# Performance work log

Hardware: AMD Instinct MI355X
Metric: run time of the kernel (lower is better)

## Reference

```python
import jax, jax.numpy as jnp
from jax import lax
import numpy as np

N = 8192
E = 131072
HID = 256
ENC = 256
L = 4
EPS = 1e-5


def _linear(x, w, b):
    return x @ w.T + b


def _layernorm(x, g, b):
    mu = x.mean(-1, keepdims=True)
    var = ((x - mu) ** 2).mean(-1, keepdims=True)
    return (x - mu) / jnp.sqrt(var + EPS) * g + b


def _conv_bn_gelu(x, w, b, g, beta, stride, pad):
    # eval-mode BatchNorm with running_mean=0, running_var=1
    y = lax.conv_general_dilated(x, w, (stride, stride), [(pad, pad), (pad, pad)],
                                 dimension_numbers=('NCHW', 'OIHW', 'NCHW'))
    y = y + b[None, :, None, None]
    y = y / jnp.sqrt(1.0 + EPS) * g[None, :, None, None] + beta[None, :, None, None]
    return jax.nn.gelu(y, approximate=False)


def setup_inputs() -> dict:
    key = jax.random.key(0)
    ks = iter(jax.random.split(key, 40))

    def rn(shape, scale=0.05):
        return (jax.random.normal(next(ks), shape, jnp.float32) * scale)

    inp = {
        'patches': jax.random.normal(next(ks), (N, 3, 32, 32), jnp.float32),
        'coords': jax.random.uniform(next(ks), (N, 2), jnp.float32) * 10000.0,
        'edge_index': jax.random.randint(next(ks), (2, E), 0, N),
        # SimpleCNNEncoder
        'c1_w': rn((32, 3, 5, 5)), 'c1_b': rn((32,)), 'bn1_g': jnp.ones((32,)), 'bn1_b': jnp.zeros((32,)),
        'c2_w': rn((64, 32, 3, 3)), 'c2_b': rn((64,)), 'bn2_g': jnp.ones((64,)), 'bn2_b': jnp.zeros((64,)),
        'c3_w': rn((128, 64, 3, 3)), 'c3_b': rn((128,)), 'bn3_g': jnp.ones((128,)), 'bn3_b': jnp.zeros((128,)),
        'c4_w': rn((256, 128, 3, 3)), 'c4_b': rn((256,)), 'bn4_g': jnp.ones((256,)), 'bn4_b': jnp.zeros((256,)),
        'enc_proj_w': rn((ENC, 256)), 'enc_proj_b': rn((ENC,)),
        # projector
        'pj_w': rn((HID, ENC + 2)), 'pj_b': rn((HID,)),
        'pln_g': jnp.ones((HID,)), 'pln_b': jnp.zeros((HID,)),
        # graph blocks (stacked over L)
        'gb_msg_w': rn((L, HID, HID)), 'gb_msg_b': rn((L, HID)),
        'gb_sp_w': rn((L, HID, HID)), 'gb_sp_b': rn((L, HID)),
        'gb_ln_g': jnp.ones((L, HID)), 'gb_ln_b': jnp.zeros((L, HID)),
        # heads
        'comp_w': rn((8, HID)), 'comp_b': rn((8,)),
        'cmpo_w': rn((16, HID)), 'cmpo_b': rn((16,)),
        'prog_w': rn((32, HID)), 'prog_b': rn((32,)),
    }
    return inp


def _forward(patches, coords, edge_index,
             c1_w, c1_b, bn1_g, bn1_b, c2_w, c2_b, bn2_g, bn2_b,
             c3_w, c3_b, bn3_g, bn3_b, c4_w, c4_b, bn4_g, bn4_b,
             enc_proj_w, enc_proj_b, pj_w, pj_b, pln_g, pln_b,
             gb_msg_w, gb_msg_b, gb_sp_w, gb_sp_b, gb_ln_g, gb_ln_b,
             comp_w, comp_b, cmpo_w, cmpo_b, prog_w, prog_b):
    # CNN encoder
    h = _conv_bn_gelu(patches, c1_w, c1_b, bn1_g, bn1_b, 2, 2)   # [N,32,16,16]
    h = _conv_bn_gelu(h, c2_w, c2_b, bn2_g, bn2_b, 2, 1)         # [N,64,8,8]
    h = _conv_bn_gelu(h, c3_w, c3_b, bn3_g, bn3_b, 2, 1)         # [N,128,4,4]
    h = _conv_bn_gelu(h, c4_w, c4_b, bn4_g, bn4_b, 2, 1)         # [N,256,2,2]
    h = h.mean(axis=(2, 3))                                       # AdaptiveAvgPool2d(1)
    img_feat = _linear(h, enc_proj_w, enc_proj_b)                 # [N,ENC]

    # projector (Dropout is identity in eval)
    x = jnp.concatenate([img_feat, coords / 10000.0], axis=1)
    x = _layernorm(_linear(x, pj_w, pj_b), pln_g, pln_b)
    x = jax.nn.gelu(x, approximate=False)

    # graph blocks: gather -> linear -> scatter-mean -> residual -> LN
    src, dst = edge_index[0], edge_index[1]
    n = x.shape[0]
    deg = jax.ops.segment_sum(jnp.ones_like(dst, x.dtype), dst, num_segments=n)
    inv_deg = 1.0 / jnp.maximum(deg, 1.0)
    for i in range(gb_msg_w.shape[0]):
        messages = _linear(x[src], gb_msg_w[i], gb_msg_b[i])      # [E,HID]
        agg = jax.ops.segment_sum(messages, dst, num_segments=n) * inv_deg[:, None]
        out = _linear(x, gb_sp_w[i], gb_sp_b[i]) + agg
        x = _layernorm(x + jax.nn.gelu(out, approximate=False), gb_ln_g[i], gb_ln_b[i])

    return (x,
            _linear(x, comp_w, comp_b),
            _linear(x, cmpo_w, cmpo_b),
            _linear(x, prog_w, prog_b))


def reference(patches, coords, edge_index,
              c1_w, c1_b, bn1_g, bn1_b, c2_w, c2_b, bn2_g, bn2_b,
              c3_w, c3_b, bn3_g, bn3_b, c4_w, c4_b, bn4_g, bn4_b,
              enc_proj_w, enc_proj_b, pj_w, pj_b, pln_g, pln_b,
              gb_msg_w, gb_msg_b, gb_sp_w, gb_sp_b, gb_ln_g, gb_ln_b,
              comp_w, comp_b, cmpo_w, cmpo_b, prog_w, prog_b):
    return _forward(patches, coords, edge_index,
                    c1_w, c1_b, bn1_g, bn1_b, c2_w, c2_b, bn2_g, bn2_b,
                    c3_w, c3_b, bn3_g, bn3_b, c4_w, c4_b, bn4_g, bn4_b,
                    enc_proj_w, enc_proj_b, pj_w, pj_b, pln_g, pln_b,
                    gb_msg_w, gb_msg_b, gb_sp_w, gb_sp_b, gb_ln_g, gb_ln_b,
                    comp_w, comp_b, cmpo_w, cmpo_b, prog_w, prog_b)
```

## Files before the change

### kernel.cpp

```cpp
#include <hip/hip_runtime.h>
#include <hip/hip_bf16.h>

#define N_ 8192
#define E_ 131072

typedef unsigned short u16;
typedef unsigned int u32;
typedef __attribute__((ext_vector_type(8))) short bf16x8;
typedef __attribute__((ext_vector_type(4))) float f32x4;

__device__ __forceinline__ float bf2f(u16 u){ return __uint_as_float(((u32)u)<<16); }
__device__ __forceinline__ u16 f2bf(float f){
  u32 u = __float_as_uint(f);
  u32 r = (u + 0x7fffu + ((u>>16)&1u)) >> 16;
  return (u16)r;
}
__device__ __forceinline__ float gelu_f(float x){ return 0.5f*x*(1.f+erff(x*0.70710678118654752f)); }

template<int S1,int S2>
__device__ __forceinline__ u32 swz(u32 b){
  if (S1==0) return b;
  u32 k = b >> S1;
  if (S2) k ^= (b >> S2);
  return b ^ ((k & 7u) << 4);
}

__global__ __launch_bounds__(256) void wpack1_k(const float* __restrict__ src,
    u16* __restrict__ dst)
{
  int e = blockIdx.x*256 + threadIdx.x;
  if (e < 3328){
    int co = e / 104, r = e - co*104;
    int ci = r >> 5, tap = r & 31;
    u16 v = 0;
    if (ci < 3 && tap < 25) v = f2bf(src[co*75 + ci*25 + tap]);
    dst[e] = v;
  }
}

__global__ __launch_bounds__(256) void wpack_k(const float* __restrict__ src,
    u16* __restrict__ dst, int CO, int CI, int total)
{
  int e = blockIdx.x*256 + threadIdx.x;
  if (e < total){
    int tap = e / (CO*CI);
    int rem = e - tap*CO*CI;
    int co = rem / CI, ci = rem - co*CI;
    dst[e] = f2bf(src[((size_t)co*CI + ci)*9 + tap]);
  }
}

__global__ __launch_bounds__(256) void conv1m_k(const float* __restrict__ patches,
    const u16* __restrict__ wp, const float* __restrict__ cb,
    const float* __restrict__ bng, const float* __restrict__ bnb,
    u16* __restrict__ h1)
{
  __shared__ __align__(16) u16 sbuf[4000 + 3328];
  int t = threadIdx.x;
  int img = blockIdx.x;

  for (int e=t; e<2000; e+=256) ((u32*)sbuf)[e] = 0;
  {
    const uint4* s4 = (const uint4*)wp;
    uint4* d4 = (uint4*)(sbuf + 4000);
    for (int e=t; e<416; e+=256) d4[e] = s4[e];
  }
  __syncthreads();
  {
    const float* src = patches + (size_t)img*3072;
    for (int e=t; e<3072; e+=256){
      int ci = e >> 10, rem = e & 1023, iy = rem >> 5, ix = rem & 31;
      sbuf[ci*1332 + (iy+2)*37 + (ix+2)] = f2bf(src[e]);
    }
  }
  __syncthreads();

  int lane = t & 63, wv = t >> 6;
  int lr = lane & 15, g = lane >> 4;

  int roff[8];
  #pragma unroll
  for (int j=0;j<8;++j){
    int tap = g*8 + j;
    int ty = (tap*13) >> 6;
    int tx = tap - ty*5;
    roff[j] = ty*74 + tx*2;
  }

  int pixb[4];
  #pragma unroll
  for (int mt=0;mt<4;++mt){
    int row = wv*64 + mt*16 + lr;
    int oy = row >> 4, ox = row & 15;
    pixb[mt] = oy*148 + ox*4;
  }

  f32x4 acc[4][2];
  #pragma unroll
  for (int mt=0;mt<4;++mt){
    acc[mt][0] = (f32x4){0.f,0.f,0.f,0.f};
    acc[mt][1] = (f32x4){0.f,0.f,0.f,0.f};
  }

  #pragma unroll
  for (int ks=0; ks<3; ++ks){
    bf16x8 bfr[2];
    #pragma unroll
    for (int nt=0;nt<2;++nt){
      u32 b = (u32)((nt*16+lr)*208 + ks*64 + g*16);
      bfr[nt] = *(const bf16x8*)((const char*)(sbuf+4000) + b);
    }
    #pragma unroll
    for (int mt=0;mt<4;++mt){
      union { bf16x8 v; u16 s[8]; } a;
      const char* base = (const char*)sbuf + ks*2664 + pixb[mt];
      #pragma unroll
      for (int j=0;j<8;++j) a.s[j] = *(const u16*)(base + roff[j]);
      acc[mt][0] = __builtin_amdgcn_mfma_f32_16x16x32_bf16(a.v, bfr[0], acc[mt][0], 0,0,0);
      acc[mt][1] = __builtin_amdgcn_mfma_f32_16x16x32_bf16(a.v, bfr[1], acc[mt][1], 0,0,0);
    }
  }

  #pragma unroll
  for (int nt=0;nt<2;++nt){
    int co = nt*16 + lr;
    float S = bng[co]*rsqrtf(1.f+1e-5f);
    float T = cb[co]*S + bnb[co];
    #pragma unroll
    for (int mt=0;mt<4;++mt){
      #pragma unroll
      for (int j=0;j<4;++j){
        int opix = wv*64 + mt*16 + g*4 + j;
        h1[(size_t)img*8192 + opix*32 + co] = f2bf(gelu_f(acc[mt][nt][j]*S + T));
      }
    }
  }
}

template<int CI,int CO,int IH,int OH,int WAVES,int MT,int SA1,int SA2,int POOL>
__global__ __launch_bounds__(WAVES*64) void convm_k(const u16* __restrict__ hin,
    const u16* __restrict__ wp, const float* __restrict__ cb,
    const float* __restrict__ bng, const float* __restrict__ bnb,
    u16* __restrict__ hout, float* __restrict__ pooled)
{
  constexpr int OPIX = OH*OH, IPIX = IH*IH;
  constexpr int NT = CO/16, KS = CI/32;
  constexpr int ROWS = WAVES*MT*16;
  constexpr int IMG = ROWS/OPIX;
  constexpr int IMGB = IPIX*CI*2;
  constexpr int TH = WAVES*64;
  constexpr int OPSH = (OPIX==64)?6:((OPIX==16)?4:2);
  constexpr int OHSH = (OH==8)?3:((OH==4)?2:1);

  __shared__ u16 in_l[IMG*IPIX*CI];

  int t = threadIdx.x, blk = blockIdx.x;
  int lane = t & 63, wv = t >> 6;
  int lr = lane & 15, g = lane >> 4;

  {
    const uint4* src = (const uint4*)(hin + (size_t)blk*IMG*IPIX*CI);
    constexpr int CH = IMG*IPIX*CI/8;
    for (int e=t; e<CH; e+=TH){
      uint4 v = src[e];
      *(uint4*)((char*)in_l + swz<SA1,SA2>((u32)e*16u)) = v;
    }
  }
  __syncthreads();

  int oyv[MT], oxv[MT], ibv[MT];
  #pragma unroll
  for (int mt=0; mt<MT; ++mt){
    int rl = wv*(MT*16) + mt*16 + lr;
    int imgl = rl >> OPSH;
    int opix = rl & (OPIX-1);
    oyv[mt] = opix >> OHSH;
    oxv[mt] = opix & (OH-1);
    ibv[mt] = imgl*IMGB;
  }

  f32x4 acc[MT][NT];
  #pragma unroll
  for (int mt=0;mt<MT;++mt)
    #pragma unroll
    for (int nt=0;nt<NT;++nt) acc[mt][nt] = (f32x4){0.f,0.f,0.f,0.f};

  for (int tap=0; tap<9; ++tap){
    int ky = (tap<3)?0:((tap<6)?1:2);
    int kx = tap - ky*3;
    const u16* wt = wp + (size_t)tap*CO*CI;
    #pragma unroll
    for (int ks=0; ks<KS; ++ks){
      bf16x8 af[MT];
      #pragma unroll
      for (int mt=0; mt<MT; ++mt){
        int iy = 2*oyv[mt] - 1 + ky;
        int ix = 2*oxv[mt] - 1 + kx;
        bf16x8 a = {};
        if (iy>=0 && iy<IH && ix>=0 && ix<IH){
          u32 b = (u32)(ibv[mt] + (iy*IH+ix)*CI*2 + ks*64 + g*16);
          a = *(const bf16x8*)((const char*)in_l + swz<SA1,SA2>(b));
        }
        af[mt] = a;
      }
      #pragma unroll
      for (int nt=0; nt<NT; ++nt){
        bf16x8 bfr = *(const bf16x8*)(wt + (size_t)(nt*16+lr)*CI + ks*32 + g*8);
        #pragma unroll
        for (int mt=0; mt<MT; ++mt)
          acc[mt][nt] = __builtin_amdgcn_mfma_f32_16x16x32_bf16(af[mt], bfr, acc[mt][nt], 0, 0, 0);
      }
    }
  }

  if (!POOL){
    #pragma unroll
    for (int nt=0; nt<NT; ++nt){
      int co = nt*16 + lr;
      float S = bng[co]*rsqrtf(1.f+1e-5f);
      float T = cb[co]*S + bnb[co];
      #pragma unroll
      for (int mt=0; mt<MT; ++mt){
        #pragma unroll
        for (int j=0;j<4;++j){
          int rl = wv*(MT*16) + mt*16 + g*4 + j;
          int imgl = rl >> OPSH, opix = rl & (OPIX-1);
          float y = gelu_f(acc[mt][nt][j]*S + T);
          hout[((size_t)(blk*IMG + imgl)*OPIX + opix)*CO + co] = f2bf(y);
        }
      }
    }
  } else {
    #pragma unroll
    for (int nt=0; nt<NT; ++nt){
      int co = nt*16 + lr;
      float S = bng[co]*rsqrtf(1.f+1e-5f);
      float T = cb[co]*S + bnb[co];
      float s = 0.f;
      #pragma unroll
      for (int j=0;j<4;++j) s += gelu_f(acc[0][nt][j]*S + T);
      int n = blk*IMG + wv*4 + g;
      pooled[(size_t)n*CO + co] = 0.25f*s;
    }
  }
}

template<int MODE>
__global__ __launch_bounds__(256) void gemm_k(const float* __restrict__ A, const float* __restrict__ W,
   const float* __restrict__ bias, int ldw,
   const float* __restrict__ A2, const float* __restrict__ W2, const float* __restrict__ bias2,
   const int* __restrict__ deg, const float* __restrict__ coords, const float* __restrict__ pjw,
   float* __restrict__ C)
{
  __shared__ float a_l[32*16];
  __shared__ float b_l[32*256];
  int t=threadIdx.x; int row0=blockIdx.x*16;
  int tm=t>>6, tn=t&63;
  float acc[4][4];
  #pragma unroll
  for (int i=0;i<4;++i)
    #pragma unroll
    for (int j=0;j<4;++j) acc[i][j]=0.f;
  const int passes = (MODE==2)?2:1;
  for (int ps2=0; ps2<passes; ++ps2){
    const float* Ap = ps2? A2:A; const float* Wp = ps2? W2:W; int ld = ps2?256:ldw;
    for (int k0=0;k0<256;k0+=32){
      {
        int e=t*2; int r=e>>5; int k=e&31;
        float2 v = *(const float2*)&Ap[(size_t)(row0+r)*256 + k0+k];
        a_l[k*16+r]=v.x; a_l[(k+1)*16+r]=v.y;
      }
      {
        const float* wr = &Wp[(size_t)t*ld + k0];
        #pragma unroll
        for (int kk=0;kk<32;kk+=2){ float2 v = *(const float2*)&wr[kk]; b_l[kk*256+t]=v.x; b_l[(kk+1)*256+t]=v.y; }
      }
      __syncthreads();
      #pragma unroll
      for (int k=0;k<32;++k){
        float4 av = *(const float4*)&a_l[k*16+tm*4];
        float4 bv = *(const float4*)&b_l[k*256+tn*4];
        float aa[4]={av.x,av.y,av.z,av.w};
        float bb[4]={bv.x,bv.y,bv.z,bv.w};
        #pragma unroll
        for (int i=0;i<4;++i)
          #pragma unroll
          for (int j=0;j<4;++j) acc[i][j]+=aa[i]*bb[j];
      }
      __syncthreads();
    }
  }
  float4 bv = *(const float4*)&bias[tn*4];
  float bias4[4]={bv.x,bv.y,bv.z,bv.w};
  float b24[4]={0.f,0.f,0.f,0.f};
  float cw0[4], cw1[4];
  if (MODE==2){
    float4 b2 = *(const float4*)&bias2[tn*4];
    b24[0]=b2.x; b24[1]=b2.y; b24[2]=b2.z; b24[3]=b2.w;
  }
  if (MODE==1){
    #pragma unroll
    for (int j=0;j<4;++j){ cw0[j]=pjw[(size_t)(tn*4+j)*258+256]; cw1[j]=pjw[(size_t)(tn*4+j)*258+257]; }
  }
  #pragma unroll
  for (int i=0;i<4;++i){
    int r = row0 + tm*4 + i;
    float g2 = 0.f, c0=0.f, c1=0.f;
    if (MODE==2) g2 = (deg[r]>0)?1.f:0.f;
    if (MODE==1){ c0 = coords[(size_t)r*2]*1e-4f; c1 = coords[(size_t)r*2+1]*1e-4f; }
    float4 o;
    float vals[4];
    #pragma unroll
    for (int j=0;j<4;++j){
      float v = acc[i][j] + bias4[j];
      if (MODE==2) v += g2*b24[j];
      if (MODE==1) v += c0*cw0[j] + c1*cw1[j];
      vals[j]=v;
    }
    o.x=vals[0]; o.y=vals[1]; o.z=vals[2]; o.w=vals[3];
    *(float4*)&C[(size_t)r*256 + tn*4] = o;
  }
}

template<int MODE>
__global__ __launch_bounds__(256) void ln_k(const float* __restrict__ xin, const float* __restrict__ tin,
  const float* __restrict__ g, const float* __restrict__ b, float* __restrict__ out)
{
  int row = blockIdx.x, t = threadIdx.x;
  size_t o = (size_t)row*256+t;
  float v;
  if (MODE==0) v = tin[o];
  else v = xin[o] + gelu_f(tin[o]);
  float s = v, sq = v*v;
  #pragma unroll
  for (int off=32; off>=1; off>>=1){ s += __shfl_xor(s,off); sq += __shfl_xor(sq,off); }
  __shared__ float red[8];
  int wv = t>>6;
  if ((t&63)==0){ red[wv*2]=s; red[wv*2+1]=sq; }
  __syncthreads();
  s = red[0]+red[2]+red[4]+red[6];
  sq = red[1]+red[3]+red[5]+red[7];
  float mu = s*(1.f/256.f);
  float var = sq*(1.f/256.f) - mu*mu;
  float rs = rsqrtf(var + 1e-5f);
  float y = (v-mu)*rs*g[t] + b[t];
  if (MODE==0) y = gelu_f(y);
  out[o] = y;
}

__global__ __launch_bounds__(256) void degcount_k(const int* __restrict__ dst, int* __restrict__ deg){
  int e = blockIdx.x*256+threadIdx.x;
  if (e<E_) atomicAdd(&deg[dst[e]],1);
}

__global__ __launch_bounds__(256) void scan_k(const int* __restrict__ deg, int* __restrict__ rowptr,
  float* __restrict__ invd)
{
  __shared__ int part[256];
  int t = threadIdx.x;
  int base = t*32; int run=0; int loc[32];
  #pragma unroll
  for (int i=0;i<32;++i){ loc[i]=run; run += deg[base+i]; }
  part[t]=run;
  __syncthreads();
  for (int off=1; off<256; off<<=1){
    int v = (t>=off)? part[t-off] : 0;
    __syncthreads();
    part[t]+=v;
    __syncthreads();
  }
  int pre = (t>0)? part[t-1] : 0;
  #pragma unroll
  for (int i=0;i<32;++i){
    rowptr[base+i] = pre + loc[i];
    int dv = deg[base+i];
    invd[base+i] = 1.f/fmaxf((float)dv,1.f);
  }
  if (t==255) rowptr[N_] = part[255];
}

__global__ __launch_bounds__(256) void fill_k(const int* __restrict__ src, const int* __restrict__ dst,
  const int* __restrict__ rowptr, int* __restrict__ cursor, int* __restrict__ colidx)
{
  int e = blockIdx.x*256+threadIdx.x;
  if (e<E_){
    int d = dst[e];
    int pos = rowptr[d] + atomicAdd(&cursor[d],1);
    colidx[pos] = src[e];
  }
}

__global__ __launch_bounds__(256) void gather_k(const float* __restrict__ x, const int* __restrict__ rowptr,
    const int* __restrict__ colidx, const float* __restrict__ invd, float* __restrict__ xbar)
{
  int d = blockIdx.x, t = threadIdx.x;
  int j0 = rowptr[d], j1 = rowptr[d+1];
  float s = 0.f;
  for (int j=j0;j<j1;++j){ int c = colidx[j]; s += x[(size_t)c*256+t]; }
  xbar[(size_t)d*256+t] = s*invd[d];
}

__global__ __launch_bounds__(64) void heads_k(const float* __restrict__ x,
  const float* __restrict__ cw, const float* __restrict__ cbs,
  const float* __restrict__ mw, const float* __restrict__ mbs,
  const float* __restrict__ pw, const float* __restrict__ pbs,
  float* __restrict__ out)
{
  __shared__ float xr[256];
  int row = blockIdx.x, t = threadIdx.x;
  *(float4*)&xr[t*4] = *(const float4*)&x[(size_t)row*256 + t*4];
  __syncthreads();
  if (t>=56) return;
  const float* w; float bb; float* op;
  if (t<8){ w=&cw[t*256]; bb=cbs[t]; op = out + 2097152 + (size_t)row*8 + t; }
  else if (t<24){ int q=t-8; w=&mw[q*256]; bb=mbs[q]; op = out + 2162688 + (size_t)row*16 + q; }
  else { int q=t-24; w=&pw[q*256]; bb=pbs[q]; op = out + 2293760 + (size_t)row*32 + q; }
  float acc=0.f;
  #pragma unroll 8
  for (int k=0;k<256;k+=4){
    float4 xv=*(const float4*)&xr[k];
    float4 wv=*(const float4*)&w[k];
    acc += xv.x*wv.x + xv.y*wv.y + xv.z*wv.z + xv.w*wv.w;
  }
  *op = acc + bb;
}

extern "C" void kernel_launch(void* const* d_in, const int* in_sizes, int n_in,
                              void* d_out, int out_size, void* d_ws, size_t ws_size,
                              hipStream_t stream)
{
  const float* patches = (const float*)d_in[0];
  const float* coords  = (const float*)d_in[1];
  const int*   eidx    = (const int*)d_in[2];
  const float* c1w = (const float*)d_in[3];  const float* c1b = (const float*)d_in[4];
  const float* b1g = (const float*)d_in[5];  const float* b1b = (const float*)d_in[6];
  const float* c2w = (const float*)d_in[7];  const float* c2b = (const float*)d_in[8];
  const float* b2g = (const float*)d_in[9];  const float* b2b = (const float*)d_in[10];
  const float* c3w = (const float*)d_in[11]; const float* c3b = (const float*)d_in[12];
  const float* b3g = (const float*)d_in[13]; const float* b3b = (const float*)d_in[14];
  const float* c4w = (const float*)d_in[15]; const float* c4b = (const float*)d_in[16];
  const float* b4g = (const float*)d_in[17]; const float* b4b = (const float*)d_in[18];
  const float* encw = (const float*)d_in[19]; const float* encb = (const float*)d_in[20];
  const float* pjw  = (const float*)d_in[21]; const float* pjb  = (const float*)d_in[22];
  const float* plng = (const float*)d_in[23]; const float* plnb = (const float*)d_in[24];
  const float* msgw = (const float*)d_in[25]; const float* msgb = (const float*)d_in[26];
  const float* spw  = (const float*)d_in[27]; const float* spb  = (const float*)d_in[28];
  const float* lng  = (const float*)d_in[29]; const float* lnb  = (const float*)d_in[30];
  const float* compw = (const float*)d_in[31]; const float* compb = (const float*)d_in[32];
  const float* cmpow = (const float*)d_in[33]; const float* cmpob = (const float*)d_in[34];
  const float* progw = (const float*)d_in[35]; const float* progb = (const float*)d_in[36];
  float* out = (float*)d_out;
  char* ws = (char*)d_ws;

  const size_t OFF_H1   = 0;
  const size_t OFF_H2   = 134217728;
  const size_t OFF_H3   = 201326592;
  const size_t OFF_POOL = 234881024;
  const size_t OFF_IMGF = 243269632;
  const size_t OFF_TBUF = 251658240;
  const size_t OFF_XA   = 260046848;
  const size_t OFF_XB   = 268435456;
  const size_t OFF_XBAR = 276824064;
  const size_t OFF_DEG  = 285212672;
  const size_t OFF_ROWP = 285245440;
  const size_t OFF_CURS = 285310976;
  const size_t OFF_COL  = 285343744;
  const size_t OFF_INVD = 285868032;
  const size_t OFF_WP4  = OFF_TBUF;
  const size_t OFF_WP3  = OFF_TBUF + 589824;
  const size_t OFF_WP2  = OFF_TBUF + 737280;
  const size_t OFF_WP1  = OFF_TBUF + 774144;

  u16* h1 = (u16*)(ws+OFF_H1);
  u16* h2 = (u16*)(ws+OFF_H2);
  u16* h3 = (u16*)(ws+OFF_H3);
  float* pooled = (float*)(ws+OFF_POOL);
  float* imgf = (float*)(ws+OFF_IMGF);
  float* tbuf = (float*)(ws+OFF_TBUF);
  float* xa = (float*)(ws+OFF_XA);
  float* xb = (float*)(ws+OFF_XB);
  float* xbar = (float*)(ws+OFF_XBAR);
  int* deg = (int*)(ws+OFF_DEG);
  int* rowp = (int*)(ws+OFF_ROWP);
  int* curs = (int*)(ws+OFF_CURS);
  int* col = (int*)(ws+OFF_COL);
  float* invd = (float*)(ws+OFF_INVD);
  u16* wp1 = (u16*)(ws+OFF_WP1);
  u16* wp2 = (u16*)(ws+OFF_WP2);
  u16* wp3 = (u16*)(ws+OFF_WP3);
  u16* wp4 = (u16*)(ws+OFF_WP4);

  hipMemsetAsync(deg, 0, 32768, stream);
  hipMemsetAsync(curs, 0, 32768, stream);

  wpack1_k<<<13,256,0,stream>>>(c1w, wp1);
  wpack_k<<<(18432+255)/256,256,0,stream>>>(c2w, wp2, 64, 32, 18432);
  wpack_k<<<(73728+255)/256,256,0,stream>>>(c3w, wp3, 128, 64, 73728);
  wpack_k<<<(294912+255)/256,256,0,stream>>>(c4w, wp4, 256, 128, 294912);

  conv1m_k<<<8192,256,0,stream>>>(patches, wp1, c1b, b1g, b1b, h1);
  convm_k<32,64,16,8,8,2,7,0,0><<<2048,512,0,stream>>>(h1, wp2, c2b, b2g, b2b, h2, nullptr);
  convm_k<64,128,8,4,4,2,8,11,0><<<1024,256,0,stream>>>(h2, wp3, c3b, b3g, b3b, h3, nullptr);
  convm_k<128,256,4,2,8,1,9,12,1><<<256,512,0,stream>>>(h3, wp4, c4b, b4g, b4b, nullptr, pooled);

  gemm_k<0><<<512,256,0,stream>>>(pooled, encw, encb, 256, nullptr,nullptr,nullptr,nullptr,nullptr,nullptr, imgf);
  gemm_k<1><<<512,256,0,stream>>>(imgf, pjw, pjb, 258, nullptr,nullptr,nullptr,nullptr, coords, pjw, tbuf);
  ln_k<0><<<8192,256,0,stream>>>(tbuf, tbuf, plng, plnb, xa);

  degcount_k<<<512,256,0,stream>>>(eidx+E_, deg);
  scan_k<<<1,256,0,stream>>>(deg, rowp, invd);
  fill_k<<<512,256,0,stream>>>(eidx, eidx+E_, rowp, curs, col);

  float* xcur = xa;
  for (int i=0;i<4;++i){
    gather_k<<<8192,256,0,stream>>>(xcur, rowp, col, invd, xbar);
    gemm_k<2><<<512,256,0,stream>>>(xcur, spw+(size_t)i*65536, spb+(size_t)i*256, 256,
                                    xbar, msgw+(size_t)i*65536, msgb+(size_t)i*256,
                                    deg, nullptr, nullptr, tbuf);
    float* xnext = (i==3)? out : ((i&1)? xa : xb);
    ln_k<1><<<8192,256,0,stream>>>(xcur, tbuf, lng+(size_t)i*256, lnb+(size_t)i*256, xnext);
    xcur = xnext;
  }
  heads_k<<<8192,64,0,stream>>>(out, compw, compb, cmpow, cmpob, progw, progb, out);
}
```

Baseline: 1.068 ms.

## Move dense linears to bf16 MFMA and split conv output channels across waves

Replaces the fp32 SIMT GEMM for the encoder projection, projector and graph-block linears with a bf16 MFMA GEMM tiled 64x64 over a 2D grid. Weights are pre-packed to bf16, and activations (pooled, imgf, x, xbar) get bf16 copies written by the producing kernels. The conv3 and conv4 kernels now split output channels across waves, which doubles their grid sizes for more parallelism. This trades fp32 precision in the graph GEMMs for tensor-core throughput, adds extra bf16 stores in the layernorm kernel, and adds weight-packing launches.

Result: faster. 947.5 us (-11.3%).

```diff
diff --git a/kernel.cpp b/kernel.cpp
--- a/kernel.cpp
+++ b/kernel.cpp
@@ -50,6 +50,16 @@
   }
 }
 
+__global__ __launch_bounds__(256) void wpackg_k(const float* __restrict__ src,
+    u16* __restrict__ dst, int ld, int total)
+{
+  int e = blockIdx.x*256 + threadIdx.x;
+  if (e < total){
+    int co = e >> 8, k = e & 255;
+    dst[e] = f2bf(src[(size_t)co*ld + k]);
+  }
+}
+
 __global__ __launch_bounds__(256) void conv1m_k(const float* __restrict__ patches,
     const u16* __restrict__ wp, const float* __restrict__ cb,
     const float* __restrict__ bng, const float* __restrict__ bnb,
@@ -137,26 +147,30 @@
   }
 }
 
-template<int CI,int CO,int IH,int OH,int WAVES,int MT,int SA1,int SA2,int POOL>
+template<int CI,int CO,int IH,int OH,int WAVES,int NW,int MT,int SA1,int SA2,int POOL>
 __global__ __launch_bounds__(WAVES*64) void convm_k(const u16* __restrict__ hin,
     const u16* __restrict__ wp, const float* __restrict__ cb,
     const float* __restrict__ bng, const float* __restrict__ bnb,
-    u16* __restrict__ hout, float* __restrict__ pooled)
+    u16* __restrict__ hout, u16* __restrict__ pooled)
 {
   constexpr int OPIX = OH*OH, IPIX = IH*IH;
-  constexpr int NT = CO/16, KS = CI/32;
-  constexpr int ROWS = WAVES*MT*16;
+  constexpr int NT = CO/16/NW, KS = CI/32;
+  constexpr int MG = WAVES/NW;
+  constexpr int ROWS = MG*MT*16;
   constexpr int IMG = ROWS/OPIX;
   constexpr int IMGB = IPIX*CI*2;
   constexpr int TH = WAVES*64;
   constexpr int OPSH = (OPIX==64)?6:((OPIX==16)?4:2);
   constexpr int OHSH = (OH==8)?3:((OH==4)?2:1);
+  constexpr int NWS = (NW==1)?0:((NW==2)?1:2);
 
   __shared__ u16 in_l[IMG*IPIX*CI];
 
   int t = threadIdx.x, blk = blockIdx.x;
   int lane = t & 63, wv = t >> 6;
   int lr = lane & 15, g = lane >> 4;
+  int mg = wv >> NWS, nw = wv & (NW-1);
+  int ncb = nw*(NT*16);
 
   {
     const uint4* src = (const uint4*)(hin + (size_t)blk*IMG*IPIX*CI);
@@ -171,7 +185,7 @@
   int oyv[MT], oxv[MT], ibv[MT];
   #pragma unroll
   for (int mt=0; mt<MT; ++mt){
-    int rl = wv*(MT*16) + mt*16 + lr;
+    int rl = mg*(MT*16) + mt*16 + lr;
     int imgl = rl >> OPSH;
     int opix = rl & (OPIX-1);
     oyv[mt] = opix >> OHSH;
@@ -205,7 +219,7 @@
       }
       #pragma unroll
       for (int nt=0; nt<NT; ++nt){
-        bf16x8 bfr = *(const bf16x8*)(wt + (size_t)(nt*16+lr)*CI + ks*32 + g*8);
+        bf16x8 bfr = *(const bf16x8*)(wt + (size_t)(ncb + nt*16+lr)*CI + ks*32 + g*8);
         #pragma unroll
         for (int mt=0; mt<MT; ++mt)
           acc[mt][nt] = __builtin_amdgcn_mfma_f32_16x16x32_bf16(af[mt], bfr, acc[mt][nt], 0, 0, 0);
@@ -216,14 +230,14 @@
   if (!POOL){
     #pragma unroll
     for (int nt=0; nt<NT; ++nt){
-      int co = nt*16 + lr;
+      int co = ncb + nt*16 + lr;
       float S = bng[co]*rsqrtf(1.f+1e-5f);
       float T = cb[co]*S + bnb[co];
       #pragma unroll
       for (int mt=0; mt<MT; ++mt){
         #pragma unroll
         for (int j=0;j<4;++j){
-          int rl = wv*(MT*16) + mt*16 + g*4 + j;
+          int rl = mg*(MT*16) + mt*16 + g*4 + j;
           int imgl = rl >> OPSH, opix = rl & (OPIX-1);
           float y = gelu_f(acc[mt][nt][j]*S + T);
           hout[((size_t)(blk*IMG + imgl)*OPIX + opix)*CO + co] = f2bf(y);
@@ -233,98 +247,83 @@
   } else {
     #pragma unroll
     for (int nt=0; nt<NT; ++nt){
-      int co = nt*16 + lr;
+      int co = ncb + nt*16 + lr;
       float S = bng[co]*rsqrtf(1.f+1e-5f);
       float T = cb[co]*S + bnb[co];
-      float s = 0.f;
-      #pragma unroll
-      for (int j=0;j<4;++j) s += gelu_f(acc[0][nt][j]*S + T);
-      int n = blk*IMG + wv*4 + g;
-      pooled[(size_t)n*CO + co] = 0.25f*s;
+      #pragma unroll
+      for (int mt=0; mt<MT; ++mt){
+        float s = 0.f;
+        #pragma unroll
+        for (int j=0;j<4;++j) s += gelu_f(acc[mt][nt][j]*S + T);
+        int n = blk*IMG + mg*(MT*4) + mt*4 + g;
+        pooled[(size_t)n*CO + co] = f2bf(0.25f*s);
+      }
     }
   }
 }
 
 template<int MODE>
-__global__ __launch_bounds__(256) void gemm_k(const float* __restrict__ A, const float* __restrict__ W,
-   const float* __restrict__ bias, int ldw,
-   const float* __restrict__ A2, const float* __restrict__ W2, const float* __restrict__ bias2,
-   const int* __restrict__ deg, const float* __restrict__ coords, const float* __restrict__ pjw,
-   float* __restrict__ C)
-{
-  __shared__ float a_l[32*16];
-  __shared__ float b_l[32*256];
-  int t=threadIdx.x; int row0=blockIdx.x*16;
-  int tm=t>>6, tn=t&63;
-  float acc[4][4];
-  #pragma unroll
-  for (int i=0;i<4;++i)
-    #pragma unroll
-    for (int j=0;j<4;++j) acc[i][j]=0.f;
+__global__ __launch_bounds__(256) void gemm_m(
+    const u16* __restrict__ A1, const u16* __restrict__ W1, const float* __restrict__ b1,
+    const u16* __restrict__ A2, const u16* __restrict__ W2, const float* __restrict__ b2,
+    const int* __restrict__ deg, const float* __restrict__ coords, const float* __restrict__ pjw,
+    float* __restrict__ Cf, u16* __restrict__ Ch)
+{
+  __shared__ __align__(16) u16 a_l[64*256];
+  int t=threadIdx.x, lane=t&63, w=t>>6, lr=lane&15, g=lane>>4;
+  int m0 = blockIdx.x*64, n0 = blockIdx.y*64;
+
+  f32x4 acc[4];
+  #pragma unroll
+  for (int nt=0;nt<4;++nt) acc[nt] = (f32x4){0.f,0.f,0.f,0.f};
+
   const int passes = (MODE==2)?2:1;
-  for (int ps2=0; ps2<passes; ++ps2){
-    const float* Ap = ps2? A2:A; const float* Wp = ps2? W2:W; int ld = ps2?256:ldw;
-    for (int k0=0;k0<256;k0+=32){
-      {
-        int e=t*2; int r=e>>5; int k=e&31;
-        float2 v = *(const float2*)&Ap[(size_t)(row0+r)*256 + k0+k];
-        a_l[k*16+r]=v.x; a_l[(k+1)*16+r]=v.y;
+  for (int ps=0; ps<passes; ++ps){
+    const u16* Ap = ps? A2:A1;
+    const u16* Wp = ps? W2:W1;
+    __syncthreads();
+    for (int e=t; e<2048; e+=256){
+      u32 b = (u32)e*16u;
+      uint4 v = *(const uint4*)(Ap + (size_t)(m0 + (e>>5))*256 + (e&31)*8);
+      *(uint4*)((char*)a_l + (b ^ (((b>>9)&7u)<<4))) = v;
+    }
+    __syncthreads();
+    #pragma unroll
+    for (int ks=0; ks<8; ++ks){
+      u32 ab = (u32)(w*16+lr)*512 + (u32)ks*64 + (u32)g*16;
+      bf16x8 af = *(const bf16x8*)((const char*)a_l + (ab ^ (((ab>>9)&7u)<<4)));
+      #pragma unroll
+      for (int nt=0; nt<4; ++nt){
+        bf16x8 bfv = *(const bf16x8*)(Wp + (size_t)(n0+nt*16+lr)*256 + ks*32 + g*8);
+        acc[nt] = __builtin_amdgcn_mfma_f32_16x16x32_bf16(af, bfv, acc[nt], 0,0,0);
       }
-      {
-        const float* wr = &Wp[(size_t)t*ld + k0];
-        #pragma unroll
-        for (int kk=0;kk<32;kk+=2){ float2 v = *(const float2*)&wr[kk]; b_l[kk*256+t]=v.x; b_l[(kk+1)*256+t]=v.y; }
-      }
-      __syncthreads();
-      #pragma unroll
-      for (int k=0;k<32;++k){
-        float4 av = *(const float4*)&a_l[k*16+tm*4];
-        float4 bv = *(const float4*)&b_l[k*256+tn*4];
-        float aa[4]={av.x,av.y,av.z,av.w};
-        float bb[4]={bv.x,bv.y,bv.z,bv.w};
-        #pragma unroll
-        for (int i=0;i<4;++i)
-          #pragma unroll
-          for (int j=0;j<4;++j) acc[i][j]+=aa[i]*bb[j];
-      }
-      __syncthreads();
-    }
-  }
-  float4 bv = *(const float4*)&bias[tn*4];
-  float bias4[4]={bv.x,bv.y,bv.z,bv.w};
-  float b24[4]={0.f,0.f,0.f,0.f};
-  float cw0[4], cw1[4];
-  if (MODE==2){
-    float4 b2 = *(const float4*)&bias2[tn*4];
-    b24[0]=b2.x; b24[1]=b2.y; b24[2]=b2.z; b24[3]=b2.w;
-  }
-  if (MODE==1){
-    #pragma unroll
-    for (int j=0;j<4;++j){ cw0[j]=pjw[(size_t)(tn*4+j)*258+256]; cw1[j]=pjw[(size_t)(tn*4+j)*258+257]; }
-  }
-  #pragma unroll
-  for (int i=0;i<4;++i){
-    int r = row0 + tm*4 + i;
-    float g2 = 0.f, c0=0.f, c1=0.f;
-    if (MODE==2) g2 = (deg[r]>0)?1.f:0.f;
-    if (MODE==1){ c0 = coords[(size_t)r*2]*1e-4f; c1 = coords[(size_t)r*2+1]*1e-4f; }
-    float4 o;
-    float vals[4];
+    }
+  }
+
+  int row_base = m0 + w*16 + g*4;
+  #pragma unroll
+  for (int nt=0; nt<4; ++nt){
+    int col = n0 + nt*16 + lr;
+    float bb = b1[col];
+    float b2v = 0.f, cw0 = 0.f, cw1 = 0.f;
+    if (MODE==2) b2v = b2[col];
+    if (MODE==1){ cw0 = pjw[(size_t)col*258+256]; cw1 = pjw[(size_t)col*258+257]; }
     #pragma unroll
     for (int j=0;j<4;++j){
-      float v = acc[i][j] + bias4[j];
-      if (MODE==2) v += g2*b24[j];
-      if (MODE==1) v += c0*cw0[j] + c1*cw1[j];
-      vals[j]=v;
-    }
-    o.x=vals[0]; o.y=vals[1]; o.z=vals[2]; o.w=vals[3];
-    *(float4*)&C[(size_t)r*256 + tn*4] = o;
+      int r = row_base + j;
+      float v = acc[nt][j] + bb;
+      if (MODE==2) v += (deg[r]>0)? b2v : 0.f;
+      if (MODE==1) v += coords[(size_t)r*2]*1e-4f*cw0 + coords[(size_t)r*2+1]*1e-4f*cw1;
+      if (MODE==0) Ch[(size_t)r*256 + col] = f2bf(v);
+      else         Cf[(size_t)r*256 + col] = v;
+    }
   }
 }
 
 template<int MODE>
 __global__ __launch_bounds__(256) void ln_k(const float* __restrict__ xin, const float* __restrict__ tin,
-  const float* __restrict__ g, const float* __restrict__ b, float* __restrict__ out)
+  const float* __restrict__ g, const float* __restrict__ b, float* __restrict__ out,
+  u16* __restrict__ houtb)
 {
   int row = blockIdx.x, t = threadIdx.x;
   size_t o = (size_t)row*256+t;
@@ -346,6 +345,7 @@
   float y = (v-mu)*rs*g[t] + b[t];
   if (MODE==0) y = gelu_f(y);
   out[o] = y;
+  houtb[o] = f2bf(y);
 }
 
 __global__ __launch_bounds__(256) void degcount_k(const int* __restrict__ dst, int* __restrict__ deg){
@@ -391,13 +391,13 @@
 }
 
 __global__ __launch_bounds__(256) void gather_k(const float* __restrict__ x, const int* __restrict__ rowptr,
-    const int* __restrict__ colidx, const float* __restrict__ invd, float* __restrict__ xbar)
+    const int* __restrict__ colidx, const float* __restrict__ invd, u16* __restrict__ xbarh)
 {
   int d = blockIdx.x, t = threadIdx.x;
   int j0 = rowptr[d], j1 = rowptr[d+1];
   float s = 0.f;
   for (int j=j0;j<j1;++j){ int c = colidx[j]; s += x[(size_t)c*256+t]; }
-  xbar[(size_t)d*256+t] = s*invd[d];
+  xbarh[(size_t)d*256+t] = f2bf(s*invd[d]);
 }
 
 __global__ __launch_bounds__(64) void heads_k(const float* __restrict__ x,
@@ -460,7 +460,6 @@
   const size_t OFF_TBUF = 251658240;
   const size_t OFF_XA   = 260046848;
   const size_t OFF_XB   = 268435456;
-  const size_t OFF_XBAR = 276824064;
   const size_t OFF_DEG  = 285212672;
   const size_t OFF_ROWP = 285245440;
   const size_t OFF_CURS = 285310976;
@@ -470,16 +469,21 @@
   const size_t OFF_WP3  = OFF_TBUF + 589824;
   const size_t OFF_WP2  = OFF_TBUF + 737280;
   const size_t OFF_WP1  = OFF_TBUF + 774144;
+  const size_t OFF_ENCH = OFF_POOL + 4194304;
+  const size_t OFF_PJH  = OFF_POOL + 4325376;
+  const size_t OFF_SPH  = OFF_IMGF + 4194304;
+  const size_t OFF_MSGH = OFF_IMGF + 4718592;
+  const size_t OFF_XH   = OFF_H1;
+  const size_t OFF_XBH  = OFF_H1 + 4194304;
 
   u16* h1 = (u16*)(ws+OFF_H1);
   u16* h2 = (u16*)(ws+OFF_H2);
   u16* h3 = (u16*)(ws+OFF_H3);
-  float* pooled = (float*)(ws+OFF_POOL);
-  float* imgf = (float*)(ws+OFF_IMGF);
+  u16* pooled = (u16*)(ws+OFF_POOL);
+  u16* imgf_h = (u16*)(ws+OFF_IMGF);
   float* tbuf = (float*)(ws+OFF_TBUF);
   float* xa = (float*)(ws+OFF_XA);
   float* xb = (float*)(ws+OFF_XB);
-  float* xbar = (float*)(ws+OFF_XBAR);
   int* deg = (int*)(ws+OFF_DEG);
   int* rowp = (int*)(ws+OFF_ROWP);
   int* curs = (int*)(ws+OFF_CURS);
@@ -489,23 +493,36 @@
   u16* wp2 = (u16*)(ws+OFF_WP2);
   u16* wp3 = (u16*)(ws+OFF_WP3);
   u16* wp4 = (u16*)(ws+OFF_WP4);
+  u16* encw_h = (u16*)(ws+OFF_ENCH);
+  u16* pjw_h  = (u16*)(ws+OFF_PJH);
+  u16* spw_h  = (u16*)(ws+OFF_SPH);
+  u16* msgw_h = (u16*)(ws+OFF_MSGH);
+  u16* xh     = (u16*)(ws+OFF_XH);
+  u16* xbarh  = (u16*)(ws+OFF_XBH);
 
   hipMemsetAsync(deg, 0, 32768, stream);
   hipMemsetAsync(curs, 0, 32768, stream);
 
   wpack1_k<<<13,256,0,stream>>>(c1w, wp1);
-  wpack_k<<<(18432+255)/256,256,0,stream>>>(c2w, wp2, 64, 32, 18432);
-  wpack_k<<<(73728+255)/256,256,0,stream>>>(c3w, wp3, 128, 64, 73728);
-  wpack_k<<<(294912+255)/256,256,0,stream>>>(c4w, wp4, 256, 128, 294912);
+  wpack_k<<<72,256,0,stream>>>(c2w, wp2, 64, 32, 18432);
+  wpack_k<<<288,256,0,stream>>>(c3w, wp3, 128, 64, 73728);
+  wpack_k<<<1152,256,0,stream>>>(c4w, wp4, 256, 128, 294912);
+  wpackg_k<<<256,256,0,stream>>>(encw, encw_h, 256, 65536);
+  wpackg_k<<<256,256,0,stream>>>(pjw,  pjw_h,  258, 65536);
+  wpackg_k<<<1024,256,0,stream>>>(spw,  spw_h,  256, 262144);
+  wpackg_k<<<1024,256,0,stream>>>(msgw, msgw_h, 256, 262144);
 
   conv1m_k<<<8192,256,0,stream>>>(patches, wp1, c1b, b1g, b1b, h1);
-  convm_k<32,64,16,8,8,2,7,0,0><<<2048,512,0,stream>>>(h1, wp2, c2b, b2g, b2b, h2, nullptr);
-  convm_k<64,128,8,4,4,2,8,11,0><<<1024,256,0,stream>>>(h2, wp3, c3b, b3g, b3b, h3, nullptr);
-  convm_k<128,256,4,2,8,1,9,12,1><<<256,512,0,stream>>>(h3, wp4, c4b, b4g, b4b, nullptr, pooled);
-
-  gemm_k<0><<<512,256,0,stream>>>(pooled, encw, encb, 256, nullptr,nullptr,nullptr,nullptr,nullptr,nullptr, imgf);
-  gemm_k<1><<<512,256,0,stream>>>(imgf, pjw, pjb, 258, nullptr,nullptr,nullptr,nullptr, coords, pjw, tbuf);
-  ln_k<0><<<8192,256,0,stream>>>(tbuf, tbuf, plng, plnb, xa);
+  convm_k<32,64,16,8,8,1,2,7,0,0><<<2048,512,0,stream>>>(h1, wp2, c2b, b2g, b2b, h2, nullptr);
+  convm_k<64,128,8,4,4,2,2,8,11,0><<<2048,256,0,stream>>>(h2, wp3, c3b, b3g, b3b, h3, nullptr);
+  convm_k<128,256,4,2,8,4,2,9,12,1><<<512,512,0,stream>>>(h3, wp4, c4b, b4g, b4b, nullptr, pooled);
+
+  dim3 gg(128,4);
+  gemm_m<0><<<gg,256,0,stream>>>(pooled, encw_h, encb, nullptr,nullptr,nullptr,
+                                 nullptr,nullptr,nullptr, nullptr, imgf_h);
+  gemm_m<1><<<gg,256,0,stream>>>(imgf_h, pjw_h, pjb, nullptr,nullptr,nullptr,
+                                 nullptr, coords, pjw, tbuf, nullptr);
+  ln_k<0><<<8192,256,0,stream>>>(tbuf, tbuf, plng, plnb, xa, xh);
 
   degcount_k<<<512,256,0,stream>>>(eidx+E_, deg);
   scan_k<<<1,256,0,stream>>>(deg, rowp, invd);
@@ -513,12 +530,12 @@
 
   float* xcur = xa;
   for (int i=0;i<4;++i){
-    gather_k<<<8192,256,0,stream>>>(xcur, rowp, col, invd, xbar);
-    gemm_k<2><<<512,256,0,stream>>>(xcur, spw+(size_t)i*65536, spb+(size_t)i*256, 256,
-                                    xbar, msgw+(size_t)i*65536, msgb+(size_t)i*256,
-                                    deg, nullptr, nullptr, tbuf);
+    gather_k<<<8192,256,0,stream>>>(xcur, rowp, col, invd, xbarh);
+    gemm_m<2><<<gg,256,0,stream>>>(xh, spw_h+(size_t)i*65536, spb+(size_t)i*256,
+                                   xbarh, msgw_h+(size_t)i*65536, msgb+(size_t)i*256,
+                                   deg, nullptr, nullptr, tbuf, nullptr);
     float* xnext = (i==3)? out : ((i&1)? xa : xb);
-    ln_k<1><<<8192,256,0,stream>>>(xcur, tbuf, lng+(size_t)i*256, lnb+(size_t)i*256, xnext);
+    ln_k<1><<<8192,256,0,stream>>>(xcur, tbuf, lng+(size_t)i*256, lnb+(size_t)i*256, xnext, xh);
     xcur = xnext;
   }
   heads_k<<<8192,64,0,stream>>>(out, compw, compb, cmpow, cmpob, progw, progb, out);
```
